# Performance work log

Measured on AMD Instinct MI355X. Metric: run time of the kernel, lower is better.

Reference implementation:

```python
import jax, jax.numpy as jnp
import numpy as np

STRIDE = (1, 2, 2)
PADDING = ((2, 2), (3, 3), (3, 3))


def setup_inputs() -> dict:
    key = jax.random.key(0)
    kx, kw, kb = jax.random.split(key, 3)
    x = jax.random.normal(kx, (8, 3, 16, 112, 112), dtype=jnp.float32)
    weight = jax.random.normal(kw, (64, 3, 5, 7, 7), dtype=jnp.float32)
    bias = jax.random.normal(kb, (64,), dtype=jnp.float32)
    return {"x": x, "weight": weight, "bias": bias}


def reference(x, weight, bias):
    # NCDHW input, OIDHW weight -> NCDHW output; same math as the
    # torch module's explicit slice-multiply-sum conv3d.
    out = jax.lax.conv_general_dilated(
        x, weight,
        window_strides=STRIDE,
        padding=PADDING,
        dimension_numbers=("NCDHW", "OIDHW", "NCDHW"),
    )
    out = out + bias[None, :, None, None, None]
    return out
```

## Files before the change

kernel.cpp:

```cpp
#include <hip/hip_runtime.h>


typedef __attribute__((ext_vector_type(8))) short short8;
typedef __attribute__((ext_vector_type(4))) float f32x4;

#define CI 3
#define DI 16
#define HI 112
#define WI 112
#define CO 64
#define DO_ 16
#define HO 56
#define WO 56
#define HW_IN 12544
#define DHWO 50176

#define NROW 105
#define NROWP 108
#define NCH 27
#define TH 4
#define NPL 6
#define LR 13
#define LROWS (CI*NPL*LR)
#define LWS 144
#define XLSZ (LROWS*LWS)

__device__ __forceinline__ unsigned short f2bf(float f) {
    unsigned u = __float_as_uint(f);
    return (unsigned short)((u + 0x7FFFu + ((u >> 16) & 1u)) >> 16);
}

__global__ void prep_weights(const float* __restrict__ wgt, short8* __restrict__ wbuf) {
    const int t    = blockIdx.x * 64 + threadIdx.x;
    const int lane = t & 63;
    const int cf   = t >> 6;
    const int ch   = cf >> 2;
    const int a    = cf & 3;
    const int l15  = lane & 15;
    const int kgrp = lane >> 4;
    const int co   = a * 16 + l15;
    const int r    = ch * 4 + kgrp;
    const int rc   = (r < NROW) ? r : (NROW - 1);
    const int c    = rc / 35;
    const int kd   = (rc / 7) % 5;
    const int kh   = rc % 7;
    const float* wsrc = wgt + (((co * CI + c) * 5 + kd) * 7 + kh) * 7;
    short8 v;
    #pragma unroll
    for (int j = 0; j < 8; ++j) {
        float w = (r < NROW && j < 7) ? wsrc[j] : 0.0f;
        v[j] = (short)f2bf(w);
    }
    wbuf[(size_t)cf * 64 + lane] = v;
}

__launch_bounds__(512, 2)
__global__ void conv3d_mfma4(const float* __restrict__ x,
                             const short8* __restrict__ wbuf,
                             const float* __restrict__ bias,
                             float* __restrict__ out) {
    __shared__ unsigned short xl[XLSZ];
    __shared__ int rowg[LROWS];
    __shared__ unsigned short tabr[NROWP];

    const int tid = threadIdx.x;
    int b = blockIdx.x;
    const int ht  = b % 14;  b /= 14;
    const int ddp = b % 8;
    const int n   = b / 8;
    const int ho0 = ht * TH;
    const int dd0 = ddp * 2;

    if (tid < LROWS) {
        const int c   = tid / (NPL * LR);
        const int rem = tid - c * (NPL * LR);
        const int p   = rem / LR;
        const int rl  = rem - p * LR;
        const int din = dd0 - 2 + p;
        const int hin = 2 * ho0 - 3 + rl;
        const bool ok = ((unsigned)din < (unsigned)DI) && ((unsigned)hin < (unsigned)HI);
        rowg[tid] = ok ? ((n * CI + c) * DI + din) * HW_IN + hin * WI : -1;
    }
    if (tid < NROWP) {
        const int rc = (tid < NROW) ? tid : (NROW - 1);
        const int c  = rc / 35;
        const int kd = (rc / 7) % 5;
        const int kh = rc % 7;
        tabr[tid] = (unsigned short)(((c * NPL + kd) * LR + kh) * LWS);
    }
    __syncthreads();

    const int lane = tid & 63;
    const int wid  = tid >> 6;

    for (int row = wid; row < LROWS; row += 8) {
        const int base = rowg[row];
        unsigned short* dst = &xl[row * LWS];
        if (lane < 57) {
            float v0 = 0.0f, v1 = 0.0f;
            const int w0 = 2 * lane - 1;
            if (base >= 0) {
                if (lane >= 1)  v0 = x[base + w0];
                if (lane <= 55) v1 = x[base + w0 + 1];
            }
            unsigned pk;
            asm("v_cvt_pk_bf16_f32 %0, %1, %2" : "=v"(pk) : "v"(v0), "v"(v1));
            *reinterpret_cast<unsigned*>(&dst[2 * lane + 2]) = pk;
        } else {
            const int dw = (lane == 57) ? 0 : lane;
            *reinterpret_cast<unsigned*>(&dst[2 * dw]) = 0u;
        }
    }
    __syncthreads();

    const int ddl  = wid & 1;
    const int hoL  = wid >> 1;
    const int l15  = lane & 15;
    const int kgrp = lane >> 4;
    const int woff = ddl * (LR * LWS) + hoL * (2 * LWS);

    f32x4 acc[4][4];
    #pragma unroll
    for (int a = 0; a < 4; ++a) {
        f32x4 bv;
        #pragma unroll
        for (int r = 0; r < 4; ++r) bv[r] = bias[a * 16 + kgrp * 4 + r];
        #pragma unroll
        for (int f = 0; f < 4; ++f) acc[a][f] = bv;
    }

    const short8* wbp = wbuf + lane;
    short8 Acur[4], Anxt[4];
    #pragma unroll
    for (int a = 0; a < 4; ++a) Acur[a] = wbp[a * 64];
    int tb = (int)tabr[kgrp] + woff;

    const unsigned* xlu = reinterpret_cast<const unsigned*>(xl);

    for (int ch = 0; ch < NCH; ++ch) {
        int tbn = 0;
        if (ch + 1 < NCH) {
            tbn = (int)tabr[(ch + 1) * 4 + kgrp] + woff;
            #pragma unroll
            for (int a = 0; a < 4; ++a) Anxt[a] = wbp[((ch + 1) * 4 + a) * 64];
        }
        const unsigned* xp = xlu + (tb >> 1) + l15;
        union { unsigned u[4]; short8 s; } bx[4];
        #pragma unroll
        for (int f = 0; f < 4; ++f) {
            const unsigned* p = xp + f * 16;
            bx[f].u[0] = p[0]; bx[f].u[1] = p[1];
            bx[f].u[2] = p[2]; bx[f].u[3] = p[3];
        }
        #pragma unroll
        for (int f = 0; f < 4; ++f) {
            acc[0][f] = __builtin_amdgcn_mfma_f32_16x16x32_bf16(Acur[0], bx[f].s, acc[0][f], 0, 0, 0);
            acc[1][f] = __builtin_amdgcn_mfma_f32_16x16x32_bf16(Acur[1], bx[f].s, acc[1][f], 0, 0, 0);
            acc[2][f] = __builtin_amdgcn_mfma_f32_16x16x32_bf16(Acur[2], bx[f].s, acc[2][f], 0, 0, 0);
            acc[3][f] = __builtin_amdgcn_mfma_f32_16x16x32_bf16(Acur[3], bx[f].s, acc[3][f], 0, 0, 0);
        }
        tb = tbn;
        #pragma unroll
        for (int a = 0; a < 4; ++a) Acur[a] = Anxt[a];
    }

    const int dd = dd0 + ddl;
    const int ho = ho0 + hoL;
    #pragma unroll
    for (int f = 0; f < 4; ++f) {
        const int wo = f * 16 + l15;
        if (f < 3 || l15 < 8) {
            float* op = out + (((size_t)(n * CO) * DO_ + dd) * HO + ho) * WO + wo;
            #pragma unroll
            for (int a = 0; a < 4; ++a) {
                const int co = a * 16 + kgrp * 4;
                #pragma unroll
                for (int r = 0; r < 4; ++r)
                    op[(size_t)(co + r) * DHWO] = acc[a][f][r];
            }
        }
    }
}

extern "C" void kernel_launch(void* const* d_in, const int* in_sizes, int n_in,
                              void* d_out, int out_size, void* d_ws, size_t ws_size,
                              hipStream_t stream) {
    const float* x    = (const float*)d_in[0];
    const float* wgt  = (const float*)d_in[1];
    const float* bias = (const float*)d_in[2];
    float* out        = (float*)d_out;
    short8* wbuf      = (short8*)d_ws;

    hipLaunchKernelGGL(prep_weights, dim3(NCH * 4, 1, 1), dim3(64, 1, 1), 0, stream,
                       wgt, wbuf);

    dim3 grid(8 * 8 * 14, 1, 1);
    hipLaunchKernelGGL(conv3d_mfma4, grid, dim3(512, 1, 1), 0, stream,
                       x, wbuf, bias, out);
}
```

Measured before the change: 77.24 us.

## Pre-pad input to bf16 in workspace and stream tiles via global_load_lds

Adds a pre-pass that converts the input to a zero-padded bf16 volume in workspace. The main conv kernel then copies contiguous segments straight into LDS with global_load_lds, so the per-block fp32 gather, bounds checks and conversion go away. Tiles shrink to 2 output rows, giving more blocks and higher occupancy (launch bounds 512,4), and the MFMA loop is software-pipelined two chunks at a time. The cost is an extra kernel launch plus a full write and re-read of the padded input. It falls back to the old kernel when the workspace is too small.

```diff
diff --git a/kernel.cpp b/kernel.cpp
--- a/kernel.cpp
+++ b/kernel.cpp
@@ -16,18 +16,43 @@
 #define DHWO 50176
 
 #define NROW 105
-#define NROWP 108
 #define NCH 27
-#define TH 4
-#define NPL 6
-#define LR 13
-#define LROWS (CI*NPL*LR)
-#define LWS 144
-#define XLSZ (LROWS*LWS)
+
+#define XP_ROW 144
+#define XP_H   119
+#define XP_D   20
+#define XPAD_SHORTS (8*3*XP_D*XP_H*XP_ROW)
+#define XPAD_BYTES  (XPAD_SHORTS*2)
+#define WBUF_OFF    XPAD_BYTES
+#define WBUF_BYTES  (NCH*4*64*16)
+#define WS_NEED     (WBUF_OFF + WBUF_BYTES + 4096)
+
+#define SEG_SH 1536
 
 __device__ __forceinline__ unsigned short f2bf(float f) {
     unsigned u = __float_as_uint(f);
     return (unsigned short)((u + 0x7FFFu + ((u >> 16) & 1u)) >> 16);
+}
+
+__global__ void prep_xpad(const float* __restrict__ x, unsigned* __restrict__ xp) {
+    const int g = blockIdx.x * 256 + threadIdx.x;
+    const int dw = g % 72;
+    int r = g / 72;
+    const int hp = r % XP_H; r /= XP_H;
+    const int dp = r % XP_D; r /= XP_D;
+    const int c  = r % 3;
+    const int n  = r / 3;
+    const int din = dp - 2, hin = hp - 3;
+    const int w0  = 2 * dw - 3;
+    float v0 = 0.0f, v1 = 0.0f;
+    if ((unsigned)din < (unsigned)DI && (unsigned)hin < (unsigned)HI) {
+        const float* xr = x + ((n * CI + c) * DI + din) * HW_IN + hin * WI;
+        if ((unsigned)w0 < (unsigned)WI)       v0 = xr[w0];
+        if ((unsigned)(w0 + 1) < (unsigned)WI) v1 = xr[w0 + 1];
+    }
+    unsigned pk;
+    asm("v_cvt_pk_bf16_f32 %0, %1, %2" : "=v"(pk) : "v"(v0), "v"(v1));
+    xp[g] = pk;
 }
 
 __global__ void prep_weights(const float* __restrict__ wgt, short8* __restrict__ wbuf) {
@@ -54,48 +79,187 @@
     wbuf[(size_t)cf * 64 + lane] = v;
 }
 
+__device__ __forceinline__ int rowbase(int r) {
+    const int rc  = (r > 104) ? 104 : r;
+    const int c   = (rc >= 70) ? 2 : ((rc >= 35) ? 1 : 0);
+    const int rem = rc - c * 35;
+    const int kd  = rem / 7;
+    const int kh  = rem - kd * 7;
+    return (c * 6 + kd) * SEG_SH + kh * XP_ROW;
+}
+
+#define MFMA(A, B, C) __builtin_amdgcn_mfma_f32_16x16x32_bf16(A, B, C, 0, 0, 0)
+
+__launch_bounds__(512, 4)
+__global__ void conv3d_v6(const unsigned short* __restrict__ xpad,
+                          const short8* __restrict__ wbuf,
+                          const float* __restrict__ bias,
+                          float* __restrict__ out) {
+    __shared__ __align__(16) unsigned short xl[18 * SEG_SH];
+
+    const int tid = threadIdx.x;
+    int b = blockIdx.x;
+    const int ht  = b % 28;  b /= 28;
+    const int ddp = b & 7;
+    const int n   = b >> 3;
+    const int ho0 = ht * 2;
+    const int dd0 = ddp * 2;
+
+    const int lane = tid & 63;
+    const int wid  = tid >> 6;
+
+    {
+        const size_t nb = (size_t)(n * CI) * XP_D;
+        for (int s = wid; s < 18; s += 8) {
+            const int c = s / 6;
+            const int p = s - c * 6;
+            const char* gsrc = (const char*)(xpad +
+                ((nb + (size_t)c * XP_D + (dd0 + p)) * XP_H + 2 * ho0) * XP_ROW)
+                + lane * 16;
+            char* ldst = (char*)&xl[s * SEG_SH];
+            __builtin_amdgcn_global_load_lds(
+                (const __attribute__((address_space(1))) void*)(gsrc),
+                (__attribute__((address_space(3))) void*)(ldst), 16, 0, 0);
+            __builtin_amdgcn_global_load_lds(
+                (const __attribute__((address_space(1))) void*)(gsrc + 1024),
+                (__attribute__((address_space(3))) void*)(ldst + 1024), 16, 0, 0);
+            __builtin_amdgcn_global_load_lds(
+                (const __attribute__((address_space(1))) void*)(gsrc + 2048),
+                (__attribute__((address_space(3))) void*)(ldst + 2048), 16, 0, 0);
+        }
+    }
+    __syncthreads();
+
+    const int ddl  = wid & 1;
+    const int hoL  = (wid >> 1) & 1;
+    const int woH  = wid >> 2;
+    const int l15  = lane & 15;
+    const int kgrp = lane >> 4;
+    const int woffs = ddl * SEG_SH + hoL * (2 * XP_ROW);
+    const int spdw  = woH * 28 + l15;
+
+    f32x4 acc[4][2];
+    #pragma unroll
+    for (int a = 0; a < 4; ++a) {
+        f32x4 bv;
+        #pragma unroll
+        for (int r = 0; r < 4; ++r) bv[r] = bias[a * 16 + kgrp * 4 + r];
+        acc[a][0] = bv; acc[a][1] = bv;
+    }
+
+    const short8* wbp = wbuf + lane;
+    const unsigned* xlu = reinterpret_cast<const unsigned*>(xl);
+
+    short8 Aa[4], Ab[4];
+    union BxU { unsigned u[4]; short8 s; };
+    BxU pa0, pa1, pb0, pb1;
+
+    #pragma unroll
+    for (int a = 0; a < 4; ++a) Aa[a] = wbp[a * 64];
+    {
+        const unsigned* xp = xlu + ((rowbase(kgrp) + woffs) >> 1) + spdw;
+        #pragma unroll
+        for (int j = 0; j < 4; ++j) { pa0.u[j] = xp[j]; pa1.u[j] = xp[16 + j]; }
+    }
+
+    for (int ch = 0; ch < NCH - 1; ch += 2) {
+        #pragma unroll
+        for (int a = 0; a < 4; ++a) Ab[a] = wbp[((ch + 1) * 4 + a) * 64];
+        {
+            const unsigned* xp = xlu + ((rowbase((ch + 1) * 4 + kgrp) + woffs) >> 1) + spdw;
+            #pragma unroll
+            for (int j = 0; j < 4; ++j) { pb0.u[j] = xp[j]; pb1.u[j] = xp[16 + j]; }
+        }
+        #pragma unroll
+        for (int a = 0; a < 4; ++a) {
+            acc[a][0] = MFMA(Aa[a], pa0.s, acc[a][0]);
+            acc[a][1] = MFMA(Aa[a], pa1.s, acc[a][1]);
+        }
+        #pragma unroll
+        for (int a = 0; a < 4; ++a) Aa[a] = wbp[((ch + 2) * 4 + a) * 64];
+        {
+            const unsigned* xp = xlu + ((rowbase((ch + 2) * 4 + kgrp) + woffs) >> 1) + spdw;
+            #pragma unroll
+            for (int j = 0; j < 4; ++j) { pa0.u[j] = xp[j]; pa1.u[j] = xp[16 + j]; }
+        }
+        #pragma unroll
+        for (int a = 0; a < 4; ++a) {
+            acc[a][0] = MFMA(Ab[a], pb0.s, acc[a][0]);
+            acc[a][1] = MFMA(Ab[a], pb1.s, acc[a][1]);
+        }
+    }
+    #pragma unroll
+    for (int a = 0; a < 4; ++a) {
+        acc[a][0] = MFMA(Aa[a], pa0.s, acc[a][0]);
+        acc[a][1] = MFMA(Aa[a], pa1.s, acc[a][1]);
+    }
+
+    const int dd = dd0 + ddl;
+    const int ho = ho0 + hoL;
+    const size_t obase = ((((size_t)n * CO) * DO_ + dd) * HO + ho) * WO;
+    #pragma unroll
+    for (int f = 0; f < 2; ++f) {
+        const int wo = woH * 28 + f * 16 + l15;
+        if (f == 0 || l15 < 12) {
+            float* op = out + obase + wo;
+            #pragma unroll
+            for (int a = 0; a < 4; ++a) {
+                const int co = a * 16 + kgrp * 4;
+                #pragma unroll
+                for (int r = 0; r < 4; ++r)
+                    op[(size_t)(co + r) * DHWO] = acc[a][f][r];
+            }
+        }
+    }
+}
+
+#define FB_LR 13
+#define FB_LROWS 234
+#define FB_LWS 144
+#define FB_XLSZ (FB_LROWS*FB_LWS)
+
 __launch_bounds__(512, 2)
 __global__ void conv3d_mfma4(const float* __restrict__ x,
                              const short8* __restrict__ wbuf,
                              const float* __restrict__ bias,
                              float* __restrict__ out) {
-    __shared__ unsigned short xl[XLSZ];
-    __shared__ int rowg[LROWS];
-    __shared__ unsigned short tabr[NROWP];
+    __shared__ unsigned short xl[FB_XLSZ];
+    __shared__ int rowg[FB_LROWS];
+    __shared__ unsigned short tabr[108];
 
     const int tid = threadIdx.x;
     int b = blockIdx.x;
     const int ht  = b % 14;  b /= 14;
     const int ddp = b % 8;
     const int n   = b / 8;
-    const int ho0 = ht * TH;
+    const int ho0 = ht * 4;
     const int dd0 = ddp * 2;
 
-    if (tid < LROWS) {
-        const int c   = tid / (NPL * LR);
-        const int rem = tid - c * (NPL * LR);
-        const int p   = rem / LR;
-        const int rl  = rem - p * LR;
+    if (tid < FB_LROWS) {
+        const int c   = tid / (6 * FB_LR);
+        const int rem = tid - c * (6 * FB_LR);
+        const int p   = rem / FB_LR;
+        const int rl  = rem - p * FB_LR;
         const int din = dd0 - 2 + p;
         const int hin = 2 * ho0 - 3 + rl;
         const bool ok = ((unsigned)din < (unsigned)DI) && ((unsigned)hin < (unsigned)HI);
         rowg[tid] = ok ? ((n * CI + c) * DI + din) * HW_IN + hin * WI : -1;
     }
-    if (tid < NROWP) {
+    if (tid < 108) {
         const int rc = (tid < NROW) ? tid : (NROW - 1);
         const int c  = rc / 35;
         const int kd = (rc / 7) % 5;
         const int kh = rc % 7;
-        tabr[tid] = (unsigned short)(((c * NPL + kd) * LR + kh) * LWS);
+        tabr[tid] = (unsigned short)(((c * 6 + kd) * FB_LR + kh) * FB_LWS);
     }
     __syncthreads();
 
     const int lane = tid & 63;
     const int wid  = tid >> 6;
 
-    for (int row = wid; row < LROWS; row += 8) {
+    for (int row = wid; row < FB_LROWS; row += 8) {
         const int base = rowg[row];
-        unsigned short* dst = &xl[row * LWS];
+        unsigned short* dst = &xl[row * FB_LWS];
         if (lane < 57) {
             float v0 = 0.0f, v1 = 0.0f;
             const int w0 = 2 * lane - 1;
@@ -117,7 +281,7 @@
     const int hoL  = wid >> 1;
     const int l15  = lane & 15;
     const int kgrp = lane >> 4;
-    const int woff = ddl * (LR * LWS) + hoL * (2 * LWS);
+    const int woff = ddl * (FB_LR * FB_LWS) + hoL * (2 * FB_LWS);
 
     f32x4 acc[4][4];
     #pragma unroll
@@ -154,10 +318,10 @@
         }
         #pragma unroll
         for (int f = 0; f < 4; ++f) {
-            acc[0][f] = __builtin_amdgcn_mfma_f32_16x16x32_bf16(Acur[0], bx[f].s, acc[0][f], 0, 0, 0);
-            acc[1][f] = __builtin_amdgcn_mfma_f32_16x16x32_bf16(Acur[1], bx[f].s, acc[1][f], 0, 0, 0);
-            acc[2][f] = __builtin_amdgcn_mfma_f32_16x16x32_bf16(Acur[2], bx[f].s, acc[2][f], 0, 0, 0);
-            acc[3][f] = __builtin_amdgcn_mfma_f32_16x16x32_bf16(Acur[3], bx[f].s, acc[3][f], 0, 0, 0);
+            acc[0][f] = MFMA(Acur[0], bx[f].s, acc[0][f]);
+            acc[1][f] = MFMA(Acur[1], bx[f].s, acc[1][f]);
+            acc[2][f] = MFMA(Acur[2], bx[f].s, acc[2][f]);
+            acc[3][f] = MFMA(Acur[3], bx[f].s, acc[3][f]);
         }
         tb = tbn;
         #pragma unroll
@@ -189,12 +353,21 @@
     const float* wgt  = (const float*)d_in[1];
     const float* bias = (const float*)d_in[2];
     float* out        = (float*)d_out;
-    short8* wbuf      = (short8*)d_ws;
-
-    hipLaunchKernelGGL(prep_weights, dim3(NCH * 4, 1, 1), dim3(64, 1, 1), 0, stream,
-                       wgt, wbuf);
-
-    dim3 grid(8 * 8 * 14, 1, 1);
-    hipLaunchKernelGGL(conv3d_mfma4, grid, dim3(512, 1, 1), 0, stream,
-                       x, wbuf, bias, out);
-}
+
+    if (ws_size >= (size_t)WS_NEED) {
+        unsigned* xpad = (unsigned*)d_ws;
+        short8* wbuf   = (short8*)((char*)d_ws + WBUF_OFF);
+        hipLaunchKernelGGL(prep_xpad, dim3(16065, 1, 1), dim3(256, 1, 1), 0, stream,
+                           x, xpad);
+        hipLaunchKernelGGL(prep_weights, dim3(NCH * 4, 1, 1), dim3(64, 1, 1), 0, stream,
+                           wgt, wbuf);
+        hipLaunchKernelGGL(conv3d_v6, dim3(1792, 1, 1), dim3(512, 1, 1), 0, stream,
+                           (const unsigned short*)xpad, wbuf, bias, out);
+    } else {
+        short8* wbuf = (short8*)d_ws;
+        hipLaunchKernelGGL(prep_weights, dim3(NCH * 4, 1, 1), dim3(64, 1, 1), 0, stream,
+                           wgt, wbuf);
+        hipLaunchKernelGGL(conv3d_mfma4, dim3(896, 1, 1), dim3(512, 1, 1), 0, stream,
+                           x, wbuf, bias, out);
+    }
+}
```

Result: slower. 87.23 us (+12.9%).
